# Kernel optimization log

Measured on AMD Instinct MI355X. Metric: run time of the kernel, lower is better.

The kernel has to match this reference:

```python
import jax, jax.numpy as jnp
import numpy as np

N = 262144          # number of points
NN = 16             # max_num_neighbors
K = 15              # n_kernel_points (KPConvLayer default)
C_IN, D2, C_OUT = 128, 64, 256   # down_conv_nn=[128,256] -> bottleneck d_2=256//4
GRID, SIGMA = 0.04, 1.0
POINT_INFLUENCE = GRID * SIGMA
SLOPE = 0.2         # LeakyReLU negative_slope
EPS = 1e-5          # BatchNorm1d eps


def _bn(x, g, b):
    # BatchNorm1d in training mode: per-channel batch stats (biased variance)
    m = jnp.mean(x, axis=0)
    v = jnp.var(x, axis=0)
    return g * (x - m) * jax.lax.rsqrt(v + EPS) + b


def _lrelu(x):
    return jnp.where(x >= 0, x, SLOPE * x)


def setup_inputs() -> dict:
    key = jax.random.key(0)
    ks = jax.random.split(key, 10)
    x = jax.random.normal(ks[0], (N, C_IN), jnp.float32)
    pos = jax.random.uniform(ks[1], (N, 3), jnp.float32)
    # neighbor indices; value N is the shadow neighbor (padded row)
    idx_neighboors = jax.random.randint(ks[2], (N, NN), 0, N + 1)
    K_points = jax.random.normal(ks[3], (K, 3), jnp.float32) * POINT_INFLUENCE
    W1 = jax.random.normal(ks[4], (C_IN, D2), jnp.float32) / np.sqrt(C_IN)
    g1, b1 = jnp.ones((D2,), jnp.float32), jnp.zeros((D2,), jnp.float32)
    kp_weight = jax.random.normal(ks[5], (K, D2, D2), jnp.float32) / np.sqrt(D2)
    gkp, bkp = jnp.ones((D2,), jnp.float32), jnp.zeros((D2,), jnp.float32)
    W2 = jax.random.normal(ks[6], (D2, C_OUT), jnp.float32) / np.sqrt(D2)
    g2, b2 = jnp.ones((C_OUT,), jnp.float32), jnp.zeros((C_OUT,), jnp.float32)
    Wsc = jax.random.normal(ks[7], (C_IN, C_OUT), jnp.float32) / np.sqrt(C_IN)
    return dict(x=x, pos=pos, idx_neighboors=idx_neighboors,
                W1=W1, g1=g1, b1=b1, K_points=K_points, kp_weight=kp_weight,
                gkp=gkp, bkp=bkp, W2=W2, g2=g2, b2=b2, Wsc=Wsc)


def reference(x, pos, idx_neighboors, W1, g1, b1, K_points, kp_weight,
              gkp, bkp, W2, g2, b2, Wsc):
    # unary_1: UnaryConv -> BN -> LeakyReLU (bottleneck down)
    h = _lrelu(_bn(x @ W1, g1, b1))                              # [N, D2]

    # --- KPConv (SimpleBlock.kp_conv), non-strided: query == support ---
    h_pad = jnp.concatenate([h, jnp.zeros((1, D2), h.dtype)], axis=0)
    pos_pad = jnp.concatenate([pos, jnp.full((1, 3), 1e6, pos.dtype)], axis=0)
    neigh = pos_pad[idx_neighboors] - pos[:, None, :]            # [N, NN, 3]
    diff = neigh[:, :, None, :] - K_points[None, None, :, :]     # [N, NN, K, 3]
    dist = jnp.sqrt(jnp.sum(diff * diff, axis=-1))               # [N, NN, K]
    w = jnp.clip(1.0 - dist / POINT_INFLUENCE, 0.0)              # linear KP influence
    nfeat = h_pad[idx_neighboors]                                # [N, NN, D2]
    wf = jnp.einsum('nak,nac->nkc', w, nfeat)                    # [N, K, D2]
    out = jnp.einsum('nkc,kcd->nd', wf, kp_weight)               # sum aggregation
    out = _lrelu(_bn(out, gkp, bkp))                             # BN + activation

    # unary_2: UnaryConv -> BN -> LeakyReLU (bottleneck up)
    out = _lrelu(_bn(out @ W2, g2, b2))                          # [N, C_OUT]

    # shortcut: UnaryConv only (num_inputs != num_outputs, bn truthy branch)
    return out + x @ Wsc
```

## Files before the change

kernel.cpp:

```cpp
#include <hip/hip_runtime.h>
#include <cstdint>
#include <cstddef>

#define NPTS   262144
#define NNB    16
#define NKP    15
#define CIN    128
#define D2     64
#define COUT   256
#define PINF   0.04f
#define NSLOPE 0.2f
#define BEPS   1e-5f

#define WS_BN1_SUM  0
#define WS_BN1_SQ   64
#define WS_KP_SUM   128
#define WS_KP_SQ    192
#define WS_U2_DSUM  256
#define WS_U2_DSQ   512
#define WS_PAIRCNT  768
#define WS_PTCNT    769
#define WS_FLAGS    1024
#define WS_PLIST    (1024 + NPTS)
#define WS_ZERO_END WS_PLIST
#define WS_HPRE     (WS_PLIST + NPTS)
#define WS_KPPRE    (WS_HPRE + (size_t)NPTS * D2)
#define WS_DERIV    (WS_KPPRE + (size_t)NPTS * D2)
#define D_S1   0
#define D_T1   64
#define D_SKP  128
#define D_TKP  192
#define D_ZB   256
#define D_S2   320
#define D_T2   576
#define D_BU2  832
#define D_FB   1088
#define WS_PAIRS    (WS_DERIV + 2048)

__device__ __forceinline__ float lrelu(float v) { return v >= 0.f ? v : NSLOPE * v; }

__global__ void k0_zero(float* __restrict__ ws) {
  size_t n4 = WS_ZERO_END / 4;
  float4 z = make_float4(0.f, 0.f, 0.f, 0.f);
  for (size_t i = (size_t)blockIdx.x * blockDim.x + threadIdx.x; i < n4;
       i += (size_t)gridDim.x * blockDim.x)
    ((float4*)ws)[i] = z;
}

__global__ __launch_bounds__(256) void k1_gemm(const float* __restrict__ x,
                                               const float* __restrict__ W1,
                                               const float* __restrict__ Wsc,
                                               float* __restrict__ hpre,
                                               float* __restrict__ outp,
                                               float* __restrict__ ws) {
  __shared__ __align__(16) float As[32][72];
  __shared__ __align__(16) float Bs[5][32][64];
  __shared__ float cs[16][68];
  const int t = threadIdx.x;
  const int row0 = blockIdx.x * 64;
  const int tx = t & 15, ty = t >> 4;
  float acc[5][4][4];
#pragma unroll
  for (int j5 = 0; j5 < 5; j5++)
#pragma unroll
    for (int i = 0; i < 4; i++)
#pragma unroll
      for (int j = 0; j < 4; j++) acc[j5][i][j] = 0.f;

  for (int k0 = 0; k0 < CIN; k0 += 32) {
    __syncthreads();
    {
      int r = t >> 2;
      int c = (t & 3) * 8;
      const float* src = &x[(size_t)(row0 + r) * CIN + k0 + c];
      float4 a0 = *(const float4*)src;
      float4 a1 = *(const float4*)(src + 4);
      As[c + 0][r] = a0.x; As[c + 1][r] = a0.y; As[c + 2][r] = a0.z; As[c + 3][r] = a0.w;
      As[c + 4][r] = a1.x; As[c + 5][r] = a1.y; As[c + 6][r] = a1.z; As[c + 7][r] = a1.w;
    }
    {
      int kk = t >> 3;
      int c = (t & 7) * 8;
#pragma unroll
      for (int j5 = 0; j5 < 5; j5++) {
        const float* B = (j5 == 0) ? &W1[(size_t)(k0 + kk) * D2 + c]
                                   : &Wsc[(size_t)(k0 + kk) * COUT + (j5 - 1) * 64 + c];
        float4 b0 = *(const float4*)B;
        float4 b1 = *(const float4*)(B + 4);
        *(float4*)&Bs[j5][kk][c] = b0;
        *(float4*)&Bs[j5][kk][c + 4] = b1;
      }
    }
    __syncthreads();
#pragma unroll
    for (int k = 0; k < 32; ++k) {
      float4 av = *(const float4*)&As[k][ty * 4];
      float a[4] = {av.x, av.y, av.z, av.w};
#pragma unroll
      for (int j5 = 0; j5 < 5; j5++) {
        float4 bv = *(const float4*)&Bs[j5][k][tx * 4];
        float b[4] = {bv.x, bv.y, bv.z, bv.w};
#pragma unroll
        for (int i = 0; i < 4; i++)
#pragma unroll
          for (int j = 0; j < 4; j++) acc[j5][i][j] = fmaf(a[i], b[j], acc[j5][i][j]);
      }
    }
  }
#pragma unroll
  for (int i = 0; i < 4; i++) {
    int r = row0 + ty * 4 + i;
    *(float4*)&hpre[(size_t)r * D2 + tx * 4] =
        make_float4(acc[0][i][0], acc[0][i][1], acc[0][i][2], acc[0][i][3]);
#pragma unroll
    for (int j5 = 1; j5 < 5; j5++)
      *(float4*)&outp[(size_t)r * COUT + (j5 - 1) * 64 + tx * 4] =
          make_float4(acc[j5][i][0], acc[j5][i][1], acc[j5][i][2], acc[j5][i][3]);
  }
  __syncthreads();
#pragma unroll
  for (int j = 0; j < 4; j++)
    cs[ty][tx * 4 + j] = acc[0][0][j] + acc[0][1][j] + acc[0][2][j] + acc[0][3][j];
  __syncthreads();
  if (t < 64) {
    float s = 0.f;
#pragma unroll
    for (int w = 0; w < 16; w++) s += cs[w][t];
    atomicAdd(&ws[WS_BN1_SUM + t], s);
  }
  __syncthreads();
#pragma unroll
  for (int j = 0; j < 4; j++) {
    float q = 0.f;
#pragma unroll
    for (int i = 0; i < 4; i++) q = fmaf(acc[0][i][j], acc[0][i][j], q);
    cs[ty][tx * 4 + j] = q;
  }
  __syncthreads();
  if (t < 64) {
    float q = 0.f;
#pragma unroll
    for (int w = 0; w < 16; w++) q += cs[w][t];
    atomicAdd(&ws[WS_BN1_SQ + t], q);
  }
}

__global__ void k2b_fin1(const float* __restrict__ g1, const float* __restrict__ b1,
                         float* __restrict__ ws) {
  int c = threadIdx.x;
  float m = ws[WS_BN1_SUM + c] * (1.f / NPTS);
  float v = ws[WS_BN1_SQ + c] * (1.f / NPTS) - m * m;
  float sc = g1[c] / sqrtf(v + BEPS);
  ws[WS_DERIV + D_S1 + c] = sc;
  ws[WS_DERIV + D_T1 + c] = b1[c] - m * sc;
}

__global__ __launch_bounds__(256) void k3a_filter(const int* __restrict__ idx,
                                                  const float* __restrict__ pos,
                                                  const float* __restrict__ kpts,
                                                  float* __restrict__ ws, int cap) {
  __shared__ float kp[NKP * 3];
  int t = threadIdx.x;
  if (t < NKP * 3) kp[t] = kpts[t];
  __syncthreads();
  int id = blockIdx.x * 256 + t;
  int p = id >> 4;
  int ia = idx[id];
  if (ia >= NPTS) return;
  float px = pos[p * 3 + 0], py = pos[p * 3 + 1], pz = pos[p * 3 + 2];
  float dx = pos[ia * 3 + 0] - px, dy = pos[ia * 3 + 1] - py, dz = pos[ia * 3 + 2] - pz;
  const float thr = PINF * PINF * 1.0001f;
  bool act = false;
#pragma unroll 1
  for (int k = 0; k < NKP; k++) {
    float ex = dx - kp[k * 3 + 0], ey = dy - kp[k * 3 + 1], ez = dz - kp[k * 3 + 2];
    float s = fmaf(ex, ex, fmaf(ey, ey, ez * ez));
    act = act || (s < thr);
  }
  if (act) {
    int slot = atomicAdd((int*)&ws[WS_PAIRCNT], 1);
    if (slot < cap) {
      int* pairs = (int*)&ws[WS_PAIRS];
      pairs[2 * slot] = p;
      pairs[2 * slot + 1] = ia;
    }
    int* flags = (int*)&ws[WS_FLAGS];
    if (atomicExch(&flags[p], 1) == 0) {
      int ps = atomicAdd((int*)&ws[WS_PTCNT], 1);
      ((int*)&ws[WS_PLIST])[ps] = p;
    }
  }
}

__global__ __launch_bounds__(256) void k3c_zero_active(float* __restrict__ ws) {
  const int l = threadIdx.x & 63;
  const int g = blockIdx.x * 4 + (threadIdx.x >> 6);
  const int nw = gridDim.x * 4;
  const int* plist = (const int*)&ws[WS_PLIST];
  int pcnt = ((const int*)ws)[WS_PTCNT];
  float* kppre = &ws[WS_KPPRE];
  for (int i = g; i < pcnt; i += nw) kppre[(size_t)plist[i] * D2 + l] = 0.f;
}

__global__ __launch_bounds__(256) void k3b_active(const float* __restrict__ pos,
                                                  const float* __restrict__ kpts,
                                                  const float* __restrict__ kpw,
                                                  float* __restrict__ ws, int cap) {
  __shared__ float kp[NKP * 3];
  const int t = threadIdx.x;
  if (t < NKP * 3) kp[t] = kpts[t];
  __syncthreads();
  const int l = t & 63;
  const int g = blockIdx.x * 4 + (t >> 6);
  const int nw = gridDim.x * 4;
  const int* pairs = (const int*)&ws[WS_PAIRS];
  int npairs = ((const int*)ws)[WS_PAIRCNT];
  if (npairs > cap) npairs = cap;
  const float* hpre = &ws[WS_HPRE];
  const float s1l = ws[WS_DERIV + D_S1 + l];
  const float t1l = ws[WS_DERIV + D_T1 + l];
  float* kppre = &ws[WS_KPPRE];
  const float invp = 1.f / PINF;
  const float r2 = PINF * PINF;

#pragma unroll 1
  for (int i = g; i < npairs; i += nw) {
    int p = pairs[2 * i], ia = pairs[2 * i + 1];
    float px = pos[p * 3 + 0], py = pos[p * 3 + 1], pz = pos[p * 3 + 2];
    float dx = pos[ia * 3 + 0] - px, dy = pos[ia * 3 + 1] - py, dz = pos[ia * 3 + 2] - pz;
    unsigned mask = 0;
#pragma unroll 1
    for (int k = 0; k < NKP; k++) {
      float ex = dx - kp[k * 3 + 0], ey = dy - kp[k * 3 + 1], ez = dz - kp[k * 3 + 2];
      float s = fmaf(ex, ex, fmaf(ey, ey, ez * ez));
      if (s < r2) mask |= (1u << k);
    }
    if (mask == 0) continue;
    float f = lrelu(fmaf(s1l, hpre[(size_t)ia * D2 + l], t1l));
    float accd = 0.f;
#pragma unroll 1
    while (mask) {
      int k = __ffs(mask) - 1;
      mask &= mask - 1;
      float ex = dx - kp[k * 3 + 0], ey = dy - kp[k * 3 + 1], ez = dz - kp[k * 3 + 2];
      float s = fmaf(ex, ex, fmaf(ey, ey, ez * ez));
      float wk = 1.f - sqrtf(s) * invp;
      const float* kwk = kpw + ((size_t)k << 12) + l;
      float m0 = 0.f, m1 = 0.f, m2 = 0.f, m3 = 0.f;
#pragma unroll 1
      for (int c = 0; c < D2; c += 4) {
        float f0 = __shfl(f, c + 0), f1 = __shfl(f, c + 1);
        float f2 = __shfl(f, c + 2), f3 = __shfl(f, c + 3);
        m0 = fmaf(f0, kwk[0], m0);
        m1 = fmaf(f1, kwk[64], m1);
        m2 = fmaf(f2, kwk[128], m2);
        m3 = fmaf(f3, kwk[192], m3);
        kwk += 256;
      }
      accd = fmaf(wk, (m0 + m1) + (m2 + m3), accd);
    }
    atomicAdd(&kppre[(size_t)p * D2 + l], accd);
  }
}

__global__ __launch_bounds__(256) void k4_stats_kp(float* __restrict__ ws) {
  const int t = threadIdx.x;
  const int l = t & 63, wv = t >> 6;
  const int g = blockIdx.x * 4 + wv;
  const int nw = gridDim.x * 4;
  const int* plist = (const int*)&ws[WS_PLIST];
  int pcnt = ((const int*)ws)[WS_PTCNT];
  const float* kppre = &ws[WS_KPPRE];
  float s = 0.f, q = 0.f;
  for (int i = g; i < pcnt; i += nw) {
    float v = kppre[(size_t)plist[i] * D2 + l];
    s += v;
    q = fmaf(v, v, q);
  }
  __shared__ float red[4][64];
  red[wv][l] = s;
  __syncthreads();
  if (t < 64) atomicAdd(&ws[WS_KP_SUM + t], red[0][t] + red[1][t] + red[2][t] + red[3][t]);
  __syncthreads();
  red[wv][l] = q;
  __syncthreads();
  if (t < 64) atomicAdd(&ws[WS_KP_SQ + t], red[0][t] + red[1][t] + red[2][t] + red[3][t]);
}

__global__ void k4b_fin_kp(const float* __restrict__ gkp, const float* __restrict__ bkp,
                           const float* __restrict__ W2, float* __restrict__ ws) {
  int t = threadIdx.x;
  __shared__ float zb[64];
  if (t < 64) {
    float m = ws[WS_KP_SUM + t] * (1.f / NPTS);
    float v = ws[WS_KP_SQ + t] * (1.f / NPTS) - m * m;
    float sc = gkp[t] / sqrtf(v + BEPS);
    float sh = bkp[t] - m * sc;
    ws[WS_DERIV + D_SKP + t] = sc;
    ws[WS_DERIV + D_TKP + t] = sh;
    float z = lrelu(sh);
    ws[WS_DERIV + D_ZB + t] = z;
    zb[t] = z;
  }
  __syncthreads();
  float u = 0.f;
  for (int c = 0; c < D2; c++) u = fmaf(zb[c], W2[(size_t)c * COUT + t], u);
  ws[WS_DERIV + D_BU2 + t] = u;
}

__global__ __launch_bounds__(256) void k5_stats_u2(const float* __restrict__ W2,
                                                   float* __restrict__ ws) {
  const int t = threadIdx.x;
  const int l = t & 63, wv = t >> 6;
  const int g = blockIdx.x * 4 + wv;
  const int nw = gridDim.x * 4;
  const int* plist = (const int*)&ws[WS_PLIST];
  int pcnt = ((const int*)ws)[WS_PTCNT];
  const float* kppre = &ws[WS_KPPRE];
  const float skl = ws[WS_DERIV + D_SKP + l];
  const float tkl = ws[WS_DERIV + D_TKP + l];
  float bu[4], ds[4] = {0.f, 0.f, 0.f, 0.f}, dq[4] = {0.f, 0.f, 0.f, 0.f};
#pragma unroll
  for (int j = 0; j < 4; j++) bu[j] = ws[WS_DERIV + D_BU2 + j * 64 + l];

  for (int i = g; i < pcnt; i += nw) {
    int p = plist[i];
    float z = lrelu(fmaf(skl, kppre[(size_t)p * D2 + l], tkl));
    float u0 = 0.f, u1 = 0.f, u2 = 0.f, u3 = 0.f;
#pragma unroll
    for (int c = 0; c < D2; c++) {
      float zc = __shfl(z, c);
      const float* w2c = &W2[(size_t)c * COUT + l];
      u0 = fmaf(zc, w2c[0], u0);
      u1 = fmaf(zc, w2c[64], u1);
      u2 = fmaf(zc, w2c[128], u2);
      u3 = fmaf(zc, w2c[192], u3);
    }
    float du0 = u0 - bu[0], du1 = u1 - bu[1], du2 = u2 - bu[2], du3 = u3 - bu[3];
    ds[0] += du0; ds[1] += du1; ds[2] += du2; ds[3] += du3;
    dq[0] = fmaf(du0, du0, dq[0]); dq[1] = fmaf(du1, du1, dq[1]);
    dq[2] = fmaf(du2, du2, dq[2]); dq[3] = fmaf(du3, du3, dq[3]);
  }
  __shared__ float red[4][256];
#pragma unroll
  for (int j = 0; j < 4; j++) red[wv][j * 64 + l] = ds[j];
  __syncthreads();
  atomicAdd(&ws[WS_U2_DSUM + t], red[0][t] + red[1][t] + red[2][t] + red[3][t]);
  __syncthreads();
#pragma unroll
  for (int j = 0; j < 4; j++) red[wv][j * 64 + l] = dq[j];
  __syncthreads();
  atomicAdd(&ws[WS_U2_DSQ + t], red[0][t] + red[1][t] + red[2][t] + red[3][t]);
}

__global__ void k6_fin2(const float* __restrict__ g2, const float* __restrict__ b2,
                        float* __restrict__ ws) {
  int t = threadIdx.x;
  float bu = ws[WS_DERIV + D_BU2 + t];
  float dm = ws[WS_U2_DSUM + t] * (1.f / NPTS);
  float dv = ws[WS_U2_DSQ + t] * (1.f / NPTS) - dm * dm;
  float mean = bu + dm;
  float sc = g2[t] / sqrtf(dv + BEPS);
  float sh = b2[t] - mean * sc;
  ws[WS_DERIV + D_S2 + t] = sc;
  ws[WS_DERIV + D_T2 + t] = sh;
  ws[WS_DERIV + D_FB + t] = lrelu(fmaf(sc, bu, sh));
}

__global__ __launch_bounds__(256) void k7i_inactive(float* __restrict__ out,
                                                    const float* __restrict__ ws) {
  const int* flags = (const int*)&ws[WS_FLAGS];
  const float* fb = &ws[WS_DERIV + D_FB];
  size_t n = (size_t)NPTS * 64;
  size_t stride = (size_t)gridDim.x * blockDim.x;
  for (size_t u = (size_t)blockIdx.x * blockDim.x + threadIdx.x; u < n; u += stride) {
    int r = (int)(u >> 6);
    if (flags[r]) continue;
    int s = (int)(u & 63);
    float4 o = ((float4*)out)[u];
    float4 f4 = *(const float4*)&fb[s * 4];
    o.x += f4.x; o.y += f4.y; o.z += f4.z; o.w += f4.w;
    ((float4*)out)[u] = o;
  }
}

__global__ __launch_bounds__(256) void k7a_active(const float* __restrict__ W2,
                                                  float* __restrict__ out,
                                                  float* __restrict__ ws) {
  const int t = threadIdx.x;
  const int l = t & 63;
  const int g = blockIdx.x * 4 + (t >> 6);
  const int nw = gridDim.x * 4;
  const int* plist = (const int*)&ws[WS_PLIST];
  int pcnt = ((const int*)ws)[WS_PTCNT];
  const float* kppre = &ws[WS_KPPRE];
  const float skl = ws[WS_DERIV + D_SKP + l];
  const float tkl = ws[WS_DERIV + D_TKP + l];
  float s2[4], t2[4];
#pragma unroll
  for (int j = 0; j < 4; j++) {
    s2[j] = ws[WS_DERIV + D_S2 + j * 64 + l];
    t2[j] = ws[WS_DERIV + D_T2 + j * 64 + l];
  }
  for (int i = g; i < pcnt; i += nw) {
    int p = plist[i];
    float z = lrelu(fmaf(skl, kppre[(size_t)p * D2 + l], tkl));
    float u0 = 0.f, u1 = 0.f, u2 = 0.f, u3 = 0.f;
#pragma unroll
    for (int c = 0; c < D2; c++) {
      float zc = __shfl(z, c);
      const float* w2c = &W2[(size_t)c * COUT + l];
      u0 = fmaf(zc, w2c[0], u0);
      u1 = fmaf(zc, w2c[64], u1);
      u2 = fmaf(zc, w2c[128], u2);
      u3 = fmaf(zc, w2c[192], u3);
    }
    float* op = &out[(size_t)p * COUT + l];
    op[0]   += lrelu(fmaf(s2[0], u0, t2[0]));
    op[64]  += lrelu(fmaf(s2[1], u1, t2[1]));
    op[128] += lrelu(fmaf(s2[2], u2, t2[2]));
    op[192] += lrelu(fmaf(s2[3], u3, t2[3]));
  }
}

extern "C" void kernel_launch(void* const* d_in, const int* in_sizes, int n_in,
                              void* d_out, int out_size, void* d_ws, size_t ws_size,
                              hipStream_t stream) {
  const float* x    = (const float*)d_in[0];
  const float* pos  = (const float*)d_in[1];
  const int*   idx  = (const int*)d_in[2];
  const float* W1   = (const float*)d_in[3];
  const float* g1   = (const float*)d_in[4];
  const float* b1   = (const float*)d_in[5];
  const float* kpts = (const float*)d_in[6];
  const float* kpw  = (const float*)d_in[7];
  const float* gkp  = (const float*)d_in[8];
  const float* bkp  = (const float*)d_in[9];
  const float* W2   = (const float*)d_in[10];
  const float* g2   = (const float*)d_in[11];
  const float* b2   = (const float*)d_in[12];
  const float* Wsc  = (const float*)d_in[13];
  float* out = (float*)d_out;
  float* ws = (float*)d_ws;

  long long cap_ll = ((long long)(ws_size / 4) - (long long)WS_PAIRS) / 2;
  if (cap_ll < 0) cap_ll = 0;
  if (cap_ll > (long long)NPTS * NNB) cap_ll = (long long)NPTS * NNB;
  int cap = (int)cap_ll;

  k0_zero<<<256, 256, 0, stream>>>(ws);
  k1_gemm<<<NPTS / 64, 256, 0, stream>>>(x, W1, Wsc, &ws[WS_HPRE], out, ws);
  k2b_fin1<<<1, 64, 0, stream>>>(g1, b1, ws);
  k3a_filter<<<NPTS * NNB / 256, 256, 0, stream>>>(idx, pos, kpts, ws, cap);
  k3c_zero_active<<<256, 256, 0, stream>>>(ws);
  k3b_active<<<512, 256, 0, stream>>>(pos, kpts, kpw, ws, cap);
  k4_stats_kp<<<256, 256, 0, stream>>>(ws);
  k4b_fin_kp<<<1, 256, 0, stream>>>(gkp, bkp, W2, ws);
  k5_stats_u2<<<512, 256, 0, stream>>>(W2, ws);
  k6_fin2<<<1, 256, 0, stream>>>(g2, b2, ws);
  k7i_inactive<<<2048, 256, 0, stream>>>(out, ws);
  k7a_active<<<512, 256, 0, stream>>>(W2, out, ws);
}
```

Measured before the change: 1.065 ms.

## Move shortcut GEMM to final pass fused with inactive-row bias epilogue

The shortcut GEMM x@Wsc is split out of the first GEMM and moved to the end, where it writes out plus the constant inactive-point bias directly. This removes the separate read-modify-write pass over the whole output for inactive rows. The active-point kernel now subtracts that bias to compensate. Zeroing of active kppre rows is folded into the filter kernel, dropping one launch. The cost is reading x a second time, and the first GEMM gets lighter, which should help its occupancy.

Result: faster. 1.036 ms (-2.7%).

```diff
diff --git a/kernel.cpp b/kernel.cpp
--- a/kernel.cpp
+++ b/kernel.cpp
@@ -47,25 +47,21 @@
     ((float4*)ws)[i] = z;
 }
 
-__global__ __launch_bounds__(256) void k1_gemm(const float* __restrict__ x,
-                                               const float* __restrict__ W1,
-                                               const float* __restrict__ Wsc,
-                                               float* __restrict__ hpre,
-                                               float* __restrict__ outp,
-                                               float* __restrict__ ws) {
+__global__ __launch_bounds__(256) void k1a_gemm(const float* __restrict__ x,
+                                                const float* __restrict__ W1,
+                                                float* __restrict__ hpre,
+                                                float* __restrict__ ws) {
   __shared__ __align__(16) float As[32][72];
-  __shared__ __align__(16) float Bs[5][32][64];
+  __shared__ __align__(16) float Bs[32][64];
   __shared__ float cs[16][68];
   const int t = threadIdx.x;
   const int row0 = blockIdx.x * 64;
   const int tx = t & 15, ty = t >> 4;
-  float acc[5][4][4];
-#pragma unroll
-  for (int j5 = 0; j5 < 5; j5++)
-#pragma unroll
-    for (int i = 0; i < 4; i++)
-#pragma unroll
-      for (int j = 0; j < 4; j++) acc[j5][i][j] = 0.f;
+  float acc[4][4];
+#pragma unroll
+  for (int i = 0; i < 4; i++)
+#pragma unroll
+    for (int j = 0; j < 4; j++) acc[i][j] = 0.f;
 
   for (int k0 = 0; k0 < CIN; k0 += 32) {
     __syncthreads();
@@ -81,46 +77,33 @@
     {
       int kk = t >> 3;
       int c = (t & 7) * 8;
-#pragma unroll
-      for (int j5 = 0; j5 < 5; j5++) {
-        const float* B = (j5 == 0) ? &W1[(size_t)(k0 + kk) * D2 + c]
-                                   : &Wsc[(size_t)(k0 + kk) * COUT + (j5 - 1) * 64 + c];
-        float4 b0 = *(const float4*)B;
-        float4 b1 = *(const float4*)(B + 4);
-        *(float4*)&Bs[j5][kk][c] = b0;
-        *(float4*)&Bs[j5][kk][c + 4] = b1;
-      }
+      const float* B = &W1[(size_t)(k0 + kk) * D2 + c];
+      *(float4*)&Bs[kk][c] = *(const float4*)B;
+      *(float4*)&Bs[kk][c + 4] = *(const float4*)(B + 4);
     }
     __syncthreads();
 #pragma unroll
     for (int k = 0; k < 32; ++k) {
       float4 av = *(const float4*)&As[k][ty * 4];
+      float4 bv = *(const float4*)&Bs[k][tx * 4];
       float a[4] = {av.x, av.y, av.z, av.w};
-#pragma unroll
-      for (int j5 = 0; j5 < 5; j5++) {
-        float4 bv = *(const float4*)&Bs[j5][k][tx * 4];
-        float b[4] = {bv.x, bv.y, bv.z, bv.w};
-#pragma unroll
-        for (int i = 0; i < 4; i++)
-#pragma unroll
-          for (int j = 0; j < 4; j++) acc[j5][i][j] = fmaf(a[i], b[j], acc[j5][i][j]);
-      }
+      float b[4] = {bv.x, bv.y, bv.z, bv.w};
+#pragma unroll
+      for (int i = 0; i < 4; i++)
+#pragma unroll
+        for (int j = 0; j < 4; j++) acc[i][j] = fmaf(a[i], b[j], acc[i][j]);
     }
   }
 #pragma unroll
   for (int i = 0; i < 4; i++) {
     int r = row0 + ty * 4 + i;
     *(float4*)&hpre[(size_t)r * D2 + tx * 4] =
-        make_float4(acc[0][i][0], acc[0][i][1], acc[0][i][2], acc[0][i][3]);
-#pragma unroll
-    for (int j5 = 1; j5 < 5; j5++)
-      *(float4*)&outp[(size_t)r * COUT + (j5 - 1) * 64 + tx * 4] =
-          make_float4(acc[j5][i][0], acc[j5][i][1], acc[j5][i][2], acc[j5][i][3]);
+        make_float4(acc[i][0], acc[i][1], acc[i][2], acc[i][3]);
   }
   __syncthreads();
 #pragma unroll
   for (int j = 0; j < 4; j++)
-    cs[ty][tx * 4 + j] = acc[0][0][j] + acc[0][1][j] + acc[0][2][j] + acc[0][3][j];
+    cs[ty][tx * 4 + j] = acc[0][j] + acc[1][j] + acc[2][j] + acc[3][j];
   __syncthreads();
   if (t < 64) {
     float s = 0.f;
@@ -133,7 +116,7 @@
   for (int j = 0; j < 4; j++) {
     float q = 0.f;
 #pragma unroll
-    for (int i = 0; i < 4; i++) q = fmaf(acc[0][i][j], acc[0][i][j], q);
+    for (int i = 0; i < 4; i++) q = fmaf(acc[i][j], acc[i][j], q);
     cs[ty][tx * 4 + j] = q;
   }
   __syncthreads();
@@ -188,18 +171,12 @@
     if (atomicExch(&flags[p], 1) == 0) {
       int ps = atomicAdd((int*)&ws[WS_PTCNT], 1);
       ((int*)&ws[WS_PLIST])[ps] = p;
-    }
-  }
-}
-
-__global__ __launch_bounds__(256) void k3c_zero_active(float* __restrict__ ws) {
-  const int l = threadIdx.x & 63;
-  const int g = blockIdx.x * 4 + (threadIdx.x >> 6);
-  const int nw = gridDim.x * 4;
-  const int* plist = (const int*)&ws[WS_PLIST];
-  int pcnt = ((const int*)ws)[WS_PTCNT];
-  float* kppre = &ws[WS_KPPRE];
-  for (int i = g; i < pcnt; i += nw) kppre[(size_t)plist[i] * D2 + l] = 0.f;
+      float4* row = (float4*)&ws[WS_KPPRE + (size_t)p * D2];
+      float4 z = make_float4(0.f, 0.f, 0.f, 0.f);
+#pragma unroll
+      for (int j = 0; j < 16; j++) row[j] = z;
+    }
+  }
 }
 
 __global__ __launch_bounds__(256) void k3b_active(const float* __restrict__ pos,
@@ -367,20 +344,73 @@
   ws[WS_DERIV + D_FB + t] = lrelu(fmaf(sc, bu, sh));
 }
 
-__global__ __launch_bounds__(256) void k7i_inactive(float* __restrict__ out,
-                                                    const float* __restrict__ ws) {
-  const int* flags = (const int*)&ws[WS_FLAGS];
-  const float* fb = &ws[WS_DERIV + D_FB];
-  size_t n = (size_t)NPTS * 64;
-  size_t stride = (size_t)gridDim.x * blockDim.x;
-  for (size_t u = (size_t)blockIdx.x * blockDim.x + threadIdx.x; u < n; u += stride) {
-    int r = (int)(u >> 6);
-    if (flags[r]) continue;
-    int s = (int)(u & 63);
-    float4 o = ((float4*)out)[u];
-    float4 f4 = *(const float4*)&fb[s * 4];
-    o.x += f4.x; o.y += f4.y; o.z += f4.z; o.w += f4.w;
-    ((float4*)out)[u] = o;
+__global__ __launch_bounds__(256) void k7g_gemm(const float* __restrict__ x,
+                                                const float* __restrict__ Wsc,
+                                                float* __restrict__ out,
+                                                const float* __restrict__ ws) {
+  __shared__ __align__(16) float As[32][72];
+  __shared__ __align__(16) float Bs[4][32][64];
+  const int t = threadIdx.x;
+  const int row0 = blockIdx.x * 64;
+  const int tx = t & 15, ty = t >> 4;
+  float acc[4][4][4];
+#pragma unroll
+  for (int j5 = 0; j5 < 4; j5++)
+#pragma unroll
+    for (int i = 0; i < 4; i++)
+#pragma unroll
+      for (int j = 0; j < 4; j++) acc[j5][i][j] = 0.f;
+
+  for (int k0 = 0; k0 < CIN; k0 += 32) {
+    __syncthreads();
+    {
+      int r = t >> 2;
+      int c = (t & 3) * 8;
+      const float* src = &x[(size_t)(row0 + r) * CIN + k0 + c];
+      float4 a0 = *(const float4*)src;
+      float4 a1 = *(const float4*)(src + 4);
+      As[c + 0][r] = a0.x; As[c + 1][r] = a0.y; As[c + 2][r] = a0.z; As[c + 3][r] = a0.w;
+      As[c + 4][r] = a1.x; As[c + 5][r] = a1.y; As[c + 6][r] = a1.z; As[c + 7][r] = a1.w;
+    }
+    {
+      int kk = t >> 3;
+      int c = (t & 7) * 8;
+#pragma unroll
+      for (int j5 = 0; j5 < 4; j5++) {
+        const float* B = &Wsc[(size_t)(k0 + kk) * COUT + j5 * 64 + c];
+        *(float4*)&Bs[j5][kk][c] = *(const float4*)B;
+        *(float4*)&Bs[j5][kk][c + 4] = *(const float4*)(B + 4);
+      }
+    }
+    __syncthreads();
+#pragma unroll
+    for (int k = 0; k < 32; ++k) {
+      float4 av = *(const float4*)&As[k][ty * 4];
+      float a[4] = {av.x, av.y, av.z, av.w};
+#pragma unroll
+      for (int j5 = 0; j5 < 4; j5++) {
+        float4 bv = *(const float4*)&Bs[j5][k][tx * 4];
+        float b[4] = {bv.x, bv.y, bv.z, bv.w};
+#pragma unroll
+        for (int i = 0; i < 4; i++)
+#pragma unroll
+          for (int j = 0; j < 4; j++) acc[j5][i][j] = fmaf(a[i], b[j], acc[j5][i][j]);
+      }
+    }
+  }
+  float4 fbv[4];
+#pragma unroll
+  for (int j5 = 0; j5 < 4; j5++)
+    fbv[j5] = *(const float4*)&ws[WS_DERIV + D_FB + j5 * 64 + tx * 4];
+#pragma unroll
+  for (int i = 0; i < 4; i++) {
+    int r = row0 + ty * 4 + i;
+#pragma unroll
+    for (int j5 = 0; j5 < 4; j5++) {
+      float4 o = make_float4(acc[j5][i][0] + fbv[j5].x, acc[j5][i][1] + fbv[j5].y,
+                             acc[j5][i][2] + fbv[j5].z, acc[j5][i][3] + fbv[j5].w);
+      *(float4*)&out[(size_t)r * COUT + j5 * 64 + tx * 4] = o;
+    }
   }
 }
 
@@ -396,11 +426,12 @@
   const float* kppre = &ws[WS_KPPRE];
   const float skl = ws[WS_DERIV + D_SKP + l];
   const float tkl = ws[WS_DERIV + D_TKP + l];
-  float s2[4], t2[4];
+  float s2[4], t2[4], fb[4];
 #pragma unroll
   for (int j = 0; j < 4; j++) {
     s2[j] = ws[WS_DERIV + D_S2 + j * 64 + l];
     t2[j] = ws[WS_DERIV + D_T2 + j * 64 + l];
+    fb[j] = ws[WS_DERIV + D_FB + j * 64 + l];
   }
   for (int i = g; i < pcnt; i += nw) {
     int p = plist[i];
@@ -416,10 +447,10 @@
       u3 = fmaf(zc, w2c[192], u3);
     }
     float* op = &out[(size_t)p * COUT + l];
-    op[0]   += lrelu(fmaf(s2[0], u0, t2[0]));
-    op[64]  += lrelu(fmaf(s2[1], u1, t2[1]));
-    op[128] += lrelu(fmaf(s2[2], u2, t2[2]));
-    op[192] += lrelu(fmaf(s2[3], u3, t2[3]));
+    op[0]   += lrelu(fmaf(s2[0], u0, t2[0])) - fb[0];
+    op[64]  += lrelu(fmaf(s2[1], u1, t2[1])) - fb[1];
+    op[128] += lrelu(fmaf(s2[2], u2, t2[2])) - fb[2];
+    op[192] += lrelu(fmaf(s2[3], u3, t2[3])) - fb[3];
   }
 }
 
@@ -449,15 +480,14 @@
   int cap = (int)cap_ll;
 
   k0_zero<<<256, 256, 0, stream>>>(ws);
-  k1_gemm<<<NPTS / 64, 256, 0, stream>>>(x, W1, Wsc, &ws[WS_HPRE], out, ws);
+  k1a_gemm<<<NPTS / 64, 256, 0, stream>>>(x, W1, &ws[WS_HPRE], ws);
   k2b_fin1<<<1, 64, 0, stream>>>(g1, b1, ws);
   k3a_filter<<<NPTS * NNB / 256, 256, 0, stream>>>(idx, pos, kpts, ws, cap);
-  k3c_zero_active<<<256, 256, 0, stream>>>(ws);
   k3b_active<<<512, 256, 0, stream>>>(pos, kpts, kpw, ws, cap);
   k4_stats_kp<<<256, 256, 0, stream>>>(ws);
   k4b_fin_kp<<<1, 256, 0, stream>>>(gkp, bkp, W2, ws);
   k5_stats_u2<<<512, 256, 0, stream>>>(W2, ws);
   k6_fin2<<<1, 256, 0, stream>>>(g2, b2, ws);
-  k7i_inactive<<<2048, 256, 0, stream>>>(out, ws);
+  k7g_gemm<<<NPTS / 64, 256, 0, stream>>>(x, Wsc, out, ws);
   k7a_active<<<512, 256, 0, stream>>>(W2, out, ws);
 }
```
